# Kernel tuning notes

Measured on AMD Instinct MI355X. Metric: run time of the kernel, lower is better.

## Reference

```python
import jax, jax.numpy as jnp
import numpy as np

DECAY = 0.99
EPS = 1e-06


def setup_inputs() -> dict:
    key = jax.random.key(0)
    k1, k2, k3 = jax.random.split(key, 3)
    B, S, D, K = 8, 8192, 256, 2048
    x = jax.random.normal(k1, (B, S, D), dtype=jnp.float32)
    embed = jax.random.normal(k2, (K, D), dtype=jnp.float32)
    cluster_size = jnp.ones((K,), dtype=jnp.float32)
    embed_avg = jax.random.normal(k3, (K, D), dtype=jnp.float32)
    return {"x": x, "embed": embed, "cluster_size": cluster_size, "embed_avg": embed_avg}


def reference(x, embed, cluster_size, embed_avg):
    # x: [B, S, D]; embed/embed_avg: [K, D]; cluster_size: [K]
    B, S, D = x.shape
    K = embed.shape[0]
    xf = x.reshape(-1, D)  # [N, D]
    dist = (
        jnp.sum(xf * xf, axis=1, keepdims=True)
        - 2.0 * (xf @ embed.T)
        + jnp.sum(embed * embed, axis=1)
    )
    embed_ind_flat = jnp.argmin(dist, axis=-1)  # [N]
    quantize = embed[embed_ind_flat].reshape(B, S, D)
    embed_ind = embed_ind_flat.reshape(B, S)

    # EMA updates (training branch). one_hot.sum(0) == per-code counts,
    # one_hot.T @ x == per-code feature sums; use segment_sum (no NxK one-hot).
    counts = jax.ops.segment_sum(
        jnp.ones((B * S,), dtype=jnp.float32), embed_ind_flat, num_segments=K
    )
    embed_sum = jax.ops.segment_sum(xf, embed_ind_flat, num_segments=K)  # [K, D]
    new_cluster_size = cluster_size * DECAY + (1.0 - DECAY) * counts
    new_embed_avg = embed_avg * DECAY + (1.0 - DECAY) * embed_sum
    total = new_cluster_size.sum()
    smoothed = (new_cluster_size + EPS) / (total + EPS * K) * total  # laplace smoothing
    new_embed = new_embed_avg / smoothed[:, None]
    return quantize, embed_ind, new_cluster_size, new_embed_avg, new_embed
```

## Files before the change

### kernel.cpp

```cpp
#include <hip/hip_runtime.h>
#include <hip/hip_fp16.h>
#include <float.h>

#define DECAY 0.99f
#define OMD   0.01f
#define EPSF  1e-6f

constexpr int Bb = 8, Ss = 8192, Dd = 256, Kk = 2048;
constexpr int Nn = Bb * Ss;

constexpr long OUT_QUANT = 0;
constexpr long OUT_IND   = (long)Nn * Dd;
constexpr long OUT_NCS   = OUT_IND + Nn;
constexpr long OUT_NEA   = OUT_NCS + Kk;
constexpr long OUT_NE    = OUT_NEA + (long)Kk * Dd;

constexpr long WS_COUNTS = 0;
constexpr long WS_TOTAL  = 2048;
constexpr long WS_EE     = 2112;
constexpr long WS_BIG    = 4160;
constexpr int  PARTS     = 8;
constexpr int  CODES     = 8;

typedef __attribute__((ext_vector_type(8))) short short8;
typedef __attribute__((ext_vector_type(8))) _Float16 half8;
typedef __attribute__((ext_vector_type(4))) float floatx4;

#define WINDOW 0.5f

__device__ __forceinline__ ushort f2h(float v)
{
    __half h = __float2half(v);
    return *(ushort*)&h;
}

__global__ __launch_bounds__(256) void convert_e_kernel(
    const float* __restrict__ embed, ushort* __restrict__ e_h,
    float* __restrict__ ee, int* __restrict__ qbase)
{
    if (blockIdx.x == 0 && threadIdx.x == 0) qbase[0] = 0;
    int row  = blockIdx.x * 4 + (threadIdx.x >> 6);
    int lane = threadIdx.x & 63;
    long base = (long)row * Dd + lane * 4;
    float4 v = *(const float4*)&embed[base];
    float s = v.x * v.x + v.y * v.y + v.z * v.z + v.w * v.w;
    ushort4 h;
    h.x = f2h(v.x); h.y = f2h(v.y); h.z = f2h(v.z); h.w = f2h(v.w);
    *(ushort4*)&e_h[base] = h;
    #pragma unroll
    for (int off = 32; off >= 1; off >>= 1)
        s += __shfl_xor(s, off, 64);
    if (lane == 0) ee[row] = s;
}

__global__ __attribute__((amdgpu_waves_per_eu(2, 2))) __launch_bounds__(256)
void pass1_kernel(
    const float* __restrict__ x, const ushort* __restrict__ e_h,
    const float* __restrict__ embed, const float* __restrict__ ee,
    float* __restrict__ ind_out, float* __restrict__ quant,
    int* __restrict__ qbase)
{
    __shared__ __attribute__((aligned(16))) ushort as[64 * 256];
    __shared__ float redv[4][64];
    __shared__ float red2[4][64];
    __shared__ int   redi[4][64];

    const int tid  = threadIdx.x;
    const int lane = tid & 63;
    const int quad = lane >> 4;
    const int l15  = lane & 15;
    const int w    = tid >> 6;
    const long row0 = (long)blockIdx.x * 64;

    #pragma unroll
    for (int i = 0; i < 16; ++i) {
        int li = i * 256 + tid;
        int r  = li >> 6;
        int c  = (li & 63) * 4;
        float4 v = *(const float4*)&x[row0 * Dd + (long)li * 4];
        ushort4 h;
        h.x = f2h(v.x); h.y = f2h(v.y); h.z = f2h(v.z); h.w = f2h(v.w);
        int slot = (c >> 3) ^ (r & 7);
        *(ushort4*)&as[r * 256 + slot * 8 + (c & 7)] = h;
    }
    __syncthreads();

    float bestv[16], best2v[16];
    int   besti[16];
    #pragma unroll
    for (int i = 0; i < 16; ++i) { bestv[i] = FLT_MAX; best2v[i] = FLT_MAX; besti[i] = 0; }

    for (int ct = 0; ct < Kk / 128; ++ct) {
        floatx4 acc[4][2];
        #pragma unroll
        for (int rt = 0; rt < 4; ++rt)
            #pragma unroll
            for (int jt = 0; jt < 2; ++jt)
                acc[rt][jt] = (floatx4){0.f, 0.f, 0.f, 0.f};

        const int cbase = ct * 128 + w * 32 + l15;

        #pragma unroll
        for (int ks = 0; ks < 8; ++ks) {
            half8 af[4];
            #pragma unroll
            for (int rt = 0; rt < 4; ++rt) {
                int chunk = ks * 4 + quad;
                af[rt] = *(const half8*)&as[(rt * 16 + l15) * 256 +
                                            ((chunk ^ (l15 & 7)) << 3)];
            }
            #pragma unroll
            for (int jt = 0; jt < 2; ++jt) {
                const ushort* bp = &e_h[((long)(cbase + jt * 16) << 8) +
                                        ks * 32 + quad * 8];
                half8 bf = *(const half8*)bp;
                #pragma unroll
                for (int rt = 0; rt < 4; ++rt)
                    acc[rt][jt] = __builtin_amdgcn_mfma_f32_16x16x32_f16(
                        af[rt], bf, acc[rt][jt], 0, 0, 0);
            }
        }

        #pragma unroll
        for (int jt = 0; jt < 2; ++jt) {
            int c = ct * 128 + w * 32 + jt * 16 + l15;
            float eec = ee[c];
            #pragma unroll
            for (int rt = 0; rt < 4; ++rt) {
                #pragma unroll
                for (int reg = 0; reg < 4; ++reg) {
                    float s = eec - 2.0f * acc[rt][jt][reg];
                    int slot = rt * 4 + reg;
                    if (s < bestv[slot]) {
                        best2v[slot] = bestv[slot];
                        bestv[slot] = s; besti[slot] = c;
                    } else {
                        best2v[slot] = fminf(best2v[slot], s);
                    }
                }
            }
        }
    }

    #pragma unroll
    for (int slot = 0; slot < 16; ++slot) {
        float bv = bestv[slot]; int bi = besti[slot]; float b2 = best2v[slot];
        #pragma unroll
        for (int off = 8; off >= 1; off >>= 1) {
            float ov  = __shfl_xor(bv, off, 16);
            int   oi  = __shfl_xor(bi, off, 16);
            float ov2 = __shfl_xor(b2, off, 16);
            float nm2 = fminf(fminf(b2, ov2), fmaxf(bv, ov));
            if (ov < bv) { bv = ov; bi = oi; }
            b2 = nm2;
        }
        bestv[slot] = bv; besti[slot] = bi; best2v[slot] = b2;
    }

    if (l15 == 0) {
        #pragma unroll
        for (int rt = 0; rt < 4; ++rt)
            #pragma unroll
            for (int reg = 0; reg < 4; ++reg) {
                int rloc = rt * 16 + quad * 4 + reg;
                int slot = rt * 4 + reg;
                redv[w][rloc] = bestv[slot];
                red2[w][rloc] = best2v[slot];
                redi[w][rloc] = besti[slot];
            }
    }
    __syncthreads();

    if (tid < 64) {
        float v[4], s2[4]; int ix[4];
        #pragma unroll
        for (int p = 0; p < 4; ++p) {
            v[p] = redv[p][tid]; s2[p] = red2[p][tid]; ix[p] = redi[p][tid];
        }
        float m1 = v[0]; int mi = ix[0]; int arg = 0;
        #pragma unroll
        for (int p = 1; p < 4; ++p)
            if (v[p] < m1) { m1 = v[p]; mi = ix[p]; arg = p; }
        float m2 = FLT_MAX;
        #pragma unroll
        for (int p = 0; p < 4; ++p) {
            m2 = fminf(m2, s2[p]);
            if (p != arg) m2 = fminf(m2, v[p]);
        }
        long rowAbs = row0 + tid;
        ind_out[rowAbs] = (float)mi;
        redi[0][tid] = mi;
        if (m2 - m1 <= WINDOW) {
            int q = atomicAdd(qbase, 1);
            qbase[1 + q] = (int)rowAbs;
        }
    }
    __syncthreads();

    #pragma unroll
    for (int rr = 0; rr < 16; ++rr) {
        int row = w * 16 + rr;
        int idx = redi[0][row];
        float4 ev = *(const float4*)&embed[(long)idx * Dd + lane * 4];
        *(float4*)&quant[(row0 + row) * Dd + lane * 4] = ev;
    }
}

constexpr int RB = 8;
__global__ __launch_bounds__(256) void pass2_kernel(
    const float* __restrict__ x, const float* __restrict__ embed,
    const float* __restrict__ ee, const int* __restrict__ qbase,
    float* __restrict__ ind_out, float* __restrict__ quant)
{
    __shared__ float xs[RB][256];
    __shared__ float sv[RB][256];
    __shared__ int   si[RB][256];
    const int tid = threadIdx.x;
    const int count = qbase[0];

    for (int q0 = blockIdx.x * RB; q0 < count; q0 += gridDim.x * RB) {
        const int nr = (count - q0 < RB) ? (count - q0) : RB;
        __syncthreads();
        for (int r = 0; r < nr; ++r)
            xs[r][tid] = x[(long)qbase[1 + q0 + r] * Dd + tid];
        __syncthreads();

        float bv[RB]; int bi[RB];
        #pragma unroll
        for (int r = 0; r < RB; ++r) { bv[r] = FLT_MAX; bi[r] = 0; }

        for (int i = 0; i < Kk / 256; ++i) {
            const int c = i * 256 + tid;
            const float4* er = (const float4*)&embed[(long)c * Dd];
            float dot[RB];
            #pragma unroll
            for (int r = 0; r < RB; ++r) dot[r] = 0.0f;
            for (int d = 0; d < Dd / 4; ++d) {
                float4 e4 = er[d];
                #pragma unroll
                for (int r = 0; r < RB; ++r) {
                    float4 x4 = *(const float4*)&xs[r][d * 4];
                    dot[r] += e4.x * x4.x + e4.y * x4.y + e4.z * x4.z + e4.w * x4.w;
                }
            }
            float eec = ee[c];
            #pragma unroll
            for (int r = 0; r < RB; ++r) {
                float s = eec - 2.0f * dot[r];
                if (s < bv[r]) { bv[r] = s; bi[r] = c; }
            }
        }

        #pragma unroll
        for (int r = 0; r < RB; ++r) { sv[r][tid] = bv[r]; si[r][tid] = bi[r]; }
        __syncthreads();
        for (int off = 128; off >= 1; off >>= 1) {
            if (tid < off) {
                #pragma unroll
                for (int r = 0; r < RB; ++r) {
                    float v2 = sv[r][tid + off]; int i2 = si[r][tid + off];
                    if (v2 < sv[r][tid] || (v2 == sv[r][tid] && i2 < si[r][tid])) {
                        sv[r][tid] = v2; si[r][tid] = i2;
                    }
                }
            }
            __syncthreads();
        }
        if (tid < nr)
            ind_out[qbase[1 + q0 + tid]] = (float)si[tid][0];
        for (int r = 0; r < nr; ++r) {
            int code = si[r][0];
            long row = qbase[1 + q0 + r];
            quant[row * Dd + tid] = embed[(long)code * Dd + tid];
        }
        __syncthreads();
    }
}

template <int USE_ATOMIC>
__global__ __launch_bounds__(256) void segsum_kernel(
    const float* __restrict__ x, const float* __restrict__ ind_f,
    float* __restrict__ dst, float* __restrict__ counts)
{
    __shared__ float part[CODES][4][256];
    __shared__ float cnt_l[CODES][4];
    const int tid  = threadIdx.x;
    const int w    = tid >> 6;
    const int lane = tid & 63;
    const int k0   = (blockIdx.x >> 3) * CODES;
    const int s    = blockIdx.x & 7;

    constexpr int STRIP = Nn / PARTS;
    constexpr int WAVE_ROWS = STRIP / 4;
    const int base0 = s * STRIP + w * WAVE_ROWS;

    float4 acc[CODES];
    int    cnt[CODES];
    #pragma unroll
    for (int c = 0; c < CODES; ++c) { acc[c] = (float4){0.f,0.f,0.f,0.f}; cnt[c] = 0; }

    for (int win = 0; win < WAVE_ROWS; win += 64) {
        int idx = (int)ind_f[base0 + win + lane];
        unsigned rel = (unsigned)(idx - k0);
        unsigned long long m = __ballot(rel < (unsigned)CODES);
        while (m) {
            int l = __ffsll((unsigned long long)m) - 1;
            m &= m - 1;
            int code = __shfl((int)rel, l, 64);
            long row = base0 + win + l;
            float4 v = *(const float4*)&x[row * Dd + lane * 4];
            switch (code) {
                case 0: acc[0].x+=v.x; acc[0].y+=v.y; acc[0].z+=v.z; acc[0].w+=v.w; cnt[0]++; break;
                case 1: acc[1].x+=v.x; acc[1].y+=v.y; acc[1].z+=v.z; acc[1].w+=v.w; cnt[1]++; break;
                case 2: acc[2].x+=v.x; acc[2].y+=v.y; acc[2].z+=v.z; acc[2].w+=v.w; cnt[2]++; break;
                case 3: acc[3].x+=v.x; acc[3].y+=v.y; acc[3].z+=v.z; acc[3].w+=v.w; cnt[3]++; break;
                case 4: acc[4].x+=v.x; acc[4].y+=v.y; acc[4].z+=v.z; acc[4].w+=v.w; cnt[4]++; break;
                case 5: acc[5].x+=v.x; acc[5].y+=v.y; acc[5].z+=v.z; acc[5].w+=v.w; cnt[5]++; break;
                case 6: acc[6].x+=v.x; acc[6].y+=v.y; acc[6].z+=v.z; acc[6].w+=v.w; cnt[6]++; break;
                case 7: acc[7].x+=v.x; acc[7].y+=v.y; acc[7].z+=v.z; acc[7].w+=v.w; cnt[7]++; break;
            }
        }
    }

    #pragma unroll
    for (int c = 0; c < CODES; ++c) {
        *(float4*)&part[c][w][lane * 4] = acc[c];
        if (lane == 0) cnt_l[c][w] = (float)cnt[c];
    }
    __syncthreads();

    #pragma unroll
    for (int c = 0; c < CODES; ++c) {
        float sum = part[c][0][tid] + part[c][1][tid] + part[c][2][tid] + part[c][3][tid];
        if (USE_ATOMIC) {
            if (sum != 0.0f) atomicAdd(&dst[(long)(k0 + c) * Dd + tid], sum);
        } else {
            dst[((long)s * Kk + (k0 + c)) * Dd + tid] = sum;
        }
    }
    if (tid < CODES)
        atomicAdd(&counts[k0 + tid],
                  cnt_l[tid][0] + cnt_l[tid][1] + cnt_l[tid][2] + cnt_l[tid][3]);
}

__global__ __launch_bounds__(256) void ema_cs_kernel(
    const float* __restrict__ cs, const float* __restrict__ counts,
    float* __restrict__ ncs, float* __restrict__ total_ws)
{
    __shared__ float red[256];
    int tid = threadIdx.x;
    float s = 0.0f;
    #pragma unroll
    for (int i = 0; i < 8; ++i) {
        int k = tid + i * 256;
        float v = cs[k] * DECAY + OMD * counts[k];
        ncs[k] = v;
        s += v;
    }
    red[tid] = s;
    __syncthreads();
    #pragma unroll
    for (int off = 128; off >= 1; off >>= 1) {
        if (tid < off) red[tid] += red[tid + off];
        __syncthreads();
    }
    if (tid == 0) total_ws[0] = red[0];
}

__global__ __launch_bounds__(256) void nea_ne_kernel(
    const float* __restrict__ ea, const float* __restrict__ partials,
    int nparts, const float* __restrict__ ncs, const float* __restrict__ total_ws,
    float* __restrict__ nea, float* __restrict__ ne)
{
    long g = ((long)blockIdx.x * 256 + threadIdx.x) * 4;
    int  k = (int)(g >> 8);
    int  d = (int)(g & 255);

    float4 sv = {0.f, 0.f, 0.f, 0.f};
    for (int p = 0; p < nparts; ++p) {
        float4 pv = *(const float4*)&partials[((long)p * Kk + k) * Dd + d];
        sv.x += pv.x; sv.y += pv.y; sv.z += pv.z; sv.w += pv.w;
    }

    float4 av = *(const float4*)&ea[g];
    float4 out_nea;
    out_nea.x = av.x * DECAY + OMD * sv.x;
    out_nea.y = av.y * DECAY + OMD * sv.y;
    out_nea.z = av.z * DECAY + OMD * sv.z;
    out_nea.w = av.w * DECAY + OMD * sv.w;
    *(float4*)&nea[g] = out_nea;

    float total = total_ws[0];
    float sm = (ncs[k] + EPSF) / (total + EPSF * (float)Kk) * total;
    float inv = 1.0f / sm;
    float4 out_ne;
    out_ne.x = out_nea.x * inv;
    out_ne.y = out_nea.y * inv;
    out_ne.z = out_nea.z * inv;
    out_ne.w = out_nea.w * inv;
    *(float4*)&ne[g] = out_ne;
}

extern "C" void kernel_launch(void* const* d_in, const int* in_sizes, int n_in,
                              void* d_out, int out_size, void* d_ws, size_t ws_size,
                              hipStream_t stream)
{
    const float* x     = (const float*)d_in[0];
    const float* embed = (const float*)d_in[1];
    const float* cs    = (const float*)d_in[2];
    const float* ea    = (const float*)d_in[3];

    float* out   = (float*)d_out;
    float* quant = out + OUT_QUANT;
    float* ind_f = out + OUT_IND;
    float* ncs   = out + OUT_NCS;
    float* nea   = out + OUT_NEA;
    float* ne    = out + OUT_NE;

    float* ws     = (float*)d_ws;
    float* counts = ws + WS_COUNTS;
    float* total  = ws + WS_TOTAL;
    float* ee     = ws + WS_EE;
    float* big    = ws + WS_BIG;

    ushort* e_h = (ushort*)(out + OUT_NEA);
    int*    qb  = (int*)(out + OUT_NE);

    const size_t need_partials =
        (size_t)(WS_BIG + (long)PARTS * Kk * Dd) * sizeof(float) + 1024;
    const bool use_ws_partials = ws_size >= need_partials;

    hipMemsetAsync(counts, 0, Kk * sizeof(float), stream);
    if (!use_ws_partials)
        hipMemsetAsync(big, 0, (size_t)Kk * Dd * sizeof(float), stream);

    convert_e_kernel<<<Kk / 4, 256, 0, stream>>>(embed, e_h, ee, qb);
    pass1_kernel<<<Nn / 64, 256, 0, stream>>>(x, e_h, embed, ee, ind_f, quant, qb);
    pass2_kernel<<<512, 256, 0, stream>>>(x, embed, ee, qb, ind_f, quant);
    if (use_ws_partials)
        segsum_kernel<0><<<(Kk / CODES) * PARTS, 256, 0, stream>>>(x, ind_f, big, counts);
    else
        segsum_kernel<1><<<(Kk / CODES) * PARTS, 256, 0, stream>>>(x, ind_f, big, counts);
    ema_cs_kernel<<<1, 256, 0, stream>>>(cs, counts, ncs, total);
    nea_ne_kernel<<<(Kk * Dd / 4) / 256, 256, 0, stream>>>(
        ea, big, use_ws_partials ? PARTS : 1, ncs, total, nea, ne);
}
```

Before: 447.6 us.

## Keep x fragments in registers and split codebook across waves in pass1

Pass1 drops the shared-memory staging of x. Each wave now loads its 32 rows of x straight into half8 register fragments, and the codebook is split in two halves across wave pairs, with a two-way reduction at the end. The wave occupancy hint goes from 2 to 3 per EU. Pass2's fallback distance loop is restructured so that four codes are processed per thread at once, which reuses the shared x loads across codes. The aim is to cut LDS traffic and sync and raise occupancy, at the cost of more register pressure and more redundant global reads of codebook fragments per wave.

```diff
diff --git a/kernel.cpp b/kernel.cpp
--- a/kernel.cpp
+++ b/kernel.cpp
@@ -53,97 +53,98 @@
     if (lane == 0) ee[row] = s;
 }
 
-__global__ __attribute__((amdgpu_waves_per_eu(2, 2))) __launch_bounds__(256)
+__global__ __attribute__((amdgpu_waves_per_eu(3, 3))) __launch_bounds__(256)
 void pass1_kernel(
     const float* __restrict__ x, const ushort* __restrict__ e_h,
     const float* __restrict__ embed, const float* __restrict__ ee,
     float* __restrict__ ind_out, float* __restrict__ quant,
     int* __restrict__ qbase)
 {
-    __shared__ __attribute__((aligned(16))) ushort as[64 * 256];
-    __shared__ float redv[4][64];
-    __shared__ float red2[4][64];
-    __shared__ int   redi[4][64];
+    __shared__ float redv[2][64];
+    __shared__ float red2[2][64];
+    __shared__ int   redi[2][64];
+    __shared__ int   idxs[64];
 
     const int tid  = threadIdx.x;
     const int lane = tid & 63;
     const int quad = lane >> 4;
     const int l15  = lane & 15;
     const int w    = tid >> 6;
-    const long row0 = (long)blockIdx.x * 64;
-
-    #pragma unroll
-    for (int i = 0; i < 16; ++i) {
-        int li = i * 256 + tid;
-        int r  = li >> 6;
-        int c  = (li & 63) * 4;
-        float4 v = *(const float4*)&x[row0 * Dd + (long)li * 4];
-        ushort4 h;
-        h.x = f2h(v.x); h.y = f2h(v.y); h.z = f2h(v.z); h.w = f2h(v.w);
-        int slot = (c >> 3) ^ (r & 7);
-        *(ushort4*)&as[r * 256 + slot * 8 + (c & 7)] = h;
-    }
-    __syncthreads();
-
-    float bestv[16], best2v[16];
-    int   besti[16];
-    #pragma unroll
-    for (int i = 0; i < 16; ++i) { bestv[i] = FLT_MAX; best2v[i] = FLT_MAX; besti[i] = 0; }
-
-    for (int ct = 0; ct < Kk / 128; ++ct) {
-        floatx4 acc[4][2];
-        #pragma unroll
-        for (int rt = 0; rt < 4; ++rt)
-            #pragma unroll
-            for (int jt = 0; jt < 2; ++jt)
-                acc[rt][jt] = (floatx4){0.f, 0.f, 0.f, 0.f};
-
-        const int cbase = ct * 128 + w * 32 + l15;
-
+    const int part = w & 1;
+    const int rg   = w >> 1;
+    const long row0  = (long)blockIdx.x * 64;
+    const long row0w = row0 + rg * 32;
+
+    half8 af0[8], af1[8];
+    {
+        const long ra0 = (row0w + l15) << 8;
+        const long ra1 = (row0w + 16 + l15) << 8;
         #pragma unroll
         for (int ks = 0; ks < 8; ++ks) {
-            half8 af[4];
-            #pragma unroll
-            for (int rt = 0; rt < 4; ++rt) {
-                int chunk = ks * 4 + quad;
-                af[rt] = *(const half8*)&as[(rt * 16 + l15) * 256 +
-                                            ((chunk ^ (l15 & 7)) << 3)];
-            }
-            #pragma unroll
-            for (int jt = 0; jt < 2; ++jt) {
-                const ushort* bp = &e_h[((long)(cbase + jt * 16) << 8) +
-                                        ks * 32 + quad * 8];
-                half8 bf = *(const half8*)bp;
-                #pragma unroll
-                for (int rt = 0; rt < 4; ++rt)
-                    acc[rt][jt] = __builtin_amdgcn_mfma_f32_16x16x32_f16(
-                        af[rt], bf, acc[rt][jt], 0, 0, 0);
-            }
-        }
-
-        #pragma unroll
-        for (int jt = 0; jt < 2; ++jt) {
-            int c = ct * 128 + w * 32 + jt * 16 + l15;
-            float eec = ee[c];
-            #pragma unroll
-            for (int rt = 0; rt < 4; ++rt) {
-                #pragma unroll
-                for (int reg = 0; reg < 4; ++reg) {
-                    float s = eec - 2.0f * acc[rt][jt][reg];
-                    int slot = rt * 4 + reg;
-                    if (s < bestv[slot]) {
-                        best2v[slot] = bestv[slot];
-                        bestv[slot] = s; besti[slot] = c;
-                    } else {
-                        best2v[slot] = fminf(best2v[slot], s);
-                    }
-                }
-            }
-        }
-    }
-
-    #pragma unroll
-    for (int slot = 0; slot < 16; ++slot) {
+            const int off = ks * 32 + quad * 8;
+            float4 a = *(const float4*)&x[ra0 + off];
+            float4 b = *(const float4*)&x[ra0 + off + 4];
+            half8 h;
+            h[0] = (_Float16)a.x; h[1] = (_Float16)a.y;
+            h[2] = (_Float16)a.z; h[3] = (_Float16)a.w;
+            h[4] = (_Float16)b.x; h[5] = (_Float16)b.y;
+            h[6] = (_Float16)b.z; h[7] = (_Float16)b.w;
+            af0[ks] = h;
+            float4 c = *(const float4*)&x[ra1 + off];
+            float4 d = *(const float4*)&x[ra1 + off + 4];
+            half8 g;
+            g[0] = (_Float16)c.x; g[1] = (_Float16)c.y;
+            g[2] = (_Float16)c.z; g[3] = (_Float16)c.w;
+            g[4] = (_Float16)d.x; g[5] = (_Float16)d.y;
+            g[6] = (_Float16)d.z; g[7] = (_Float16)d.w;
+            af1[ks] = g;
+        }
+    }
+
+    float bestv[8], best2v[8];
+    int   besti[8];
+    #pragma unroll
+    for (int i = 0; i < 8; ++i) { bestv[i] = FLT_MAX; best2v[i] = FLT_MAX; besti[i] = 0; }
+
+    const ushort* bbase = e_h + (((long)part * 1024 + l15) << 8) + quad * 8;
+    const float*  eeb   = ee + part * 1024 + l15;
+
+    for (int ct = 0; ct < 64; ++ct) {
+        half8 bf[8];
+        #pragma unroll
+        for (int ks = 0; ks < 8; ++ks)
+            bf[ks] = *(const half8*)&bbase[ct * 4096 + ks * 32];
+        float eec = eeb[ct * 16];
+
+        floatx4 acc0 = (floatx4){0.f, 0.f, 0.f, 0.f};
+        floatx4 acc1 = (floatx4){0.f, 0.f, 0.f, 0.f};
+        #pragma unroll
+        for (int ks = 0; ks < 8; ++ks) {
+            acc0 = __builtin_amdgcn_mfma_f32_16x16x32_f16(af0[ks], bf[ks], acc0, 0, 0, 0);
+            acc1 = __builtin_amdgcn_mfma_f32_16x16x32_f16(af1[ks], bf[ks], acc1, 0, 0, 0);
+        }
+
+        const int cc = part * 1024 + ct * 16 + l15;
+        #pragma unroll
+        for (int reg = 0; reg < 4; ++reg) {
+            float s = fmaf(-2.0f, acc0[reg], eec);
+            if (s < bestv[reg]) {
+                best2v[reg] = bestv[reg]; bestv[reg] = s; besti[reg] = cc;
+            } else {
+                best2v[reg] = fminf(best2v[reg], s);
+            }
+            float t = fmaf(-2.0f, acc1[reg], eec);
+            const int sl = 4 + reg;
+            if (t < bestv[sl]) {
+                best2v[sl] = bestv[sl]; bestv[sl] = t; besti[sl] = cc;
+            } else {
+                best2v[sl] = fminf(best2v[sl], t);
+            }
+        }
+    }
+
+    #pragma unroll
+    for (int slot = 0; slot < 8; ++slot) {
         float bv = bestv[slot]; int bi = besti[slot]; float b2 = best2v[slot];
         #pragma unroll
         for (int off = 8; off >= 1; off >>= 1) {
@@ -159,37 +160,27 @@
 
     if (l15 == 0) {
         #pragma unroll
-        for (int rt = 0; rt < 4; ++rt)
+        for (int rt = 0; rt < 2; ++rt)
             #pragma unroll
             for (int reg = 0; reg < 4; ++reg) {
-                int rloc = rt * 16 + quad * 4 + reg;
+                int r = rg * 32 + rt * 16 + quad * 4 + reg;
                 int slot = rt * 4 + reg;
-                redv[w][rloc] = bestv[slot];
-                red2[w][rloc] = best2v[slot];
-                redi[w][rloc] = besti[slot];
+                redv[part][r] = bestv[slot];
+                red2[part][r] = best2v[slot];
+                redi[part][r] = besti[slot];
             }
     }
     __syncthreads();
 
     if (tid < 64) {
-        float v[4], s2[4]; int ix[4];
-        #pragma unroll
-        for (int p = 0; p < 4; ++p) {
-            v[p] = redv[p][tid]; s2[p] = red2[p][tid]; ix[p] = redi[p][tid];
-        }
-        float m1 = v[0]; int mi = ix[0]; int arg = 0;
-        #pragma unroll
-        for (int p = 1; p < 4; ++p)
-            if (v[p] < m1) { m1 = v[p]; mi = ix[p]; arg = p; }
-        float m2 = FLT_MAX;
-        #pragma unroll
-        for (int p = 0; p < 4; ++p) {
-            m2 = fminf(m2, s2[p]);
-            if (p != arg) m2 = fminf(m2, v[p]);
-        }
+        float v0 = redv[0][tid], v1 = redv[1][tid];
+        float s0 = red2[0][tid], s1 = red2[1][tid];
+        float m1, m2; int mi;
+        if (v0 <= v1) { m1 = v0; mi = redi[0][tid]; m2 = fminf(fminf(s0, s1), v1); }
+        else          { m1 = v1; mi = redi[1][tid]; m2 = fminf(fminf(s0, s1), v0); }
         long rowAbs = row0 + tid;
         ind_out[rowAbs] = (float)mi;
-        redi[0][tid] = mi;
+        idxs[tid] = mi;
         if (m2 - m1 <= WINDOW) {
             int q = atomicAdd(qbase, 1);
             qbase[1 + q] = (int)rowAbs;
@@ -199,10 +190,10 @@
 
     #pragma unroll
     for (int rr = 0; rr < 16; ++rr) {
-        int row = w * 16 + rr;
-        int idx = redi[0][row];
+        int r = w * 16 + rr;
+        int idx = idxs[r];
         float4 ev = *(const float4*)&embed[(long)idx * Dd + lane * 4];
-        *(float4*)&quant[(row0 + row) * Dd + lane * 4] = ev;
+        *(float4*)&quant[(row0 + r) * Dd + lane * 4] = ev;
     }
 }
 
@@ -229,25 +220,38 @@
         #pragma unroll
         for (int r = 0; r < RB; ++r) { bv[r] = FLT_MAX; bi[r] = 0; }
 
-        for (int i = 0; i < Kk / 256; ++i) {
-            const int c = i * 256 + tid;
-            const float4* er = (const float4*)&embed[(long)c * Dd];
-            float dot[RB];
+        #pragma unroll
+        for (int g = 0; g < 2; ++g) {
+            float dot[RB][4];
             #pragma unroll
-            for (int r = 0; r < RB; ++r) dot[r] = 0.0f;
+            for (int r = 0; r < RB; ++r)
+                #pragma unroll
+                for (int j = 0; j < 4; ++j) dot[r][j] = 0.0f;
+
             for (int d = 0; d < Dd / 4; ++d) {
-                float4 e4 = er[d];
+                float4 xv[RB];
+                #pragma unroll
+                for (int r = 0; r < RB; ++r)
+                    xv[r] = *(const float4*)&xs[r][d * 4];
+                #pragma unroll
+                for (int j = 0; j < 4; ++j) {
+                    const int c = g * 1024 + j * 256 + tid;
+                    float4 e4 = *(const float4*)&embed[(long)c * Dd + d * 4];
+                    #pragma unroll
+                    for (int r = 0; r < RB; ++r)
+                        dot[r][j] += e4.x * xv[r].x + e4.y * xv[r].y +
+                                     e4.z * xv[r].z + e4.w * xv[r].w;
+                }
+            }
+            #pragma unroll
+            for (int j = 0; j < 4; ++j) {
+                const int c = g * 1024 + j * 256 + tid;
+                float eec = ee[c];
                 #pragma unroll
                 for (int r = 0; r < RB; ++r) {
-                    float4 x4 = *(const float4*)&xs[r][d * 4];
-                    dot[r] += e4.x * x4.x + e4.y * x4.y + e4.z * x4.z + e4.w * x4.w;
+                    float s = eec - 2.0f * dot[r][j];
+                    if (s < bv[r]) { bv[r] = s; bi[r] = c; }
                 }
-            }
-            float eec = ee[c];
-            #pragma unroll
-            for (int r = 0; r < RB; ++r) {
-                float s = eec - 2.0f * dot[r];
-                if (s < bv[r]) { bv[r] = s; bi[r] = c; }
             }
         }
 
```

New measurement: 657.6 us. 1.47x slower.

## Coalesce pass2 embed loads via quad-split dot products and shuffle-based argmin

Applied to the files above, without the earlier changes.

The fallback re-check kernel now assigns each code to four consecutive lanes, which split the 256-wide dot product and combine partials with xor shuffles. Adjacent lanes therefore read contiguous embed memory instead of striding by a whole row. The block-wide shared-memory argmin tree with many barriers becomes an in-wave shuffle reduction plus a small cross-wave merge. This adds shuffle work per code, and tie-breaking order still depends on the lowest index.

```diff
diff --git a/kernel.cpp b/kernel.cpp
--- a/kernel.cpp
+++ b/kernel.cpp
@@ -213,9 +213,14 @@
     float* __restrict__ ind_out, float* __restrict__ quant)
 {
     __shared__ float xs[RB][256];
-    __shared__ float sv[RB][256];
-    __shared__ int   si[RB][256];
-    const int tid = threadIdx.x;
+    __shared__ float mv[4][RB];
+    __shared__ int   mi[4][RB];
+    __shared__ int   fin[RB];
+    const int tid  = threadIdx.x;
+    const int w    = tid >> 6;
+    const int lane = tid & 63;
+    const int cq   = lane >> 2;
+    const int ph   = lane & 3;
     const int count = qbase[0];
 
     for (int q0 = blockIdx.x * RB; q0 < count; q0 += gridDim.x * RB) {
@@ -229,51 +234,67 @@
         #pragma unroll
         for (int r = 0; r < RB; ++r) { bv[r] = FLT_MAX; bi[r] = 0; }
 
-        for (int i = 0; i < Kk / 256; ++i) {
-            const int c = i * 256 + tid;
-            const float4* er = (const float4*)&embed[(long)c * Dd];
-            float dot[RB];
-            #pragma unroll
-            for (int r = 0; r < RB; ++r) dot[r] = 0.0f;
-            for (int d = 0; d < Dd / 4; ++d) {
-                float4 e4 = er[d];
+        for (int ch = 0; ch < 32; ++ch) {
+            const int c = w * 512 + ch * 16 + cq;
+            const float4* ep = (const float4*)&embed[(long)c * Dd + ph * 4];
+            float acc[RB];
+            #pragma unroll
+            for (int r = 0; r < RB; ++r) acc[r] = 0.0f;
+
+            #pragma unroll
+            for (int d0 = 0; d0 < 16; ++d0) {
+                float4 e4 = ep[d0 * 4];
                 #pragma unroll
                 for (int r = 0; r < RB; ++r) {
-                    float4 x4 = *(const float4*)&xs[r][d * 4];
-                    dot[r] += e4.x * x4.x + e4.y * x4.y + e4.z * x4.z + e4.w * x4.w;
+                    float4 x4 = *(const float4*)&xs[r][d0 * 16 + ph * 4];
+                    acc[r] += e4.x * x4.x + e4.y * x4.y +
+                              e4.z * x4.z + e4.w * x4.w;
                 }
             }
+            #pragma unroll
+            for (int r = 0; r < RB; ++r) {
+                acc[r] += __shfl_xor(acc[r], 1, 4);
+                acc[r] += __shfl_xor(acc[r], 2, 4);
+            }
             float eec = ee[c];
             #pragma unroll
             for (int r = 0; r < RB; ++r) {
-                float s = eec - 2.0f * dot[r];
+                float s = eec - 2.0f * acc[r];
                 if (s < bv[r]) { bv[r] = s; bi[r] = c; }
             }
         }
 
         #pragma unroll
-        for (int r = 0; r < RB; ++r) { sv[r][tid] = bv[r]; si[r][tid] = bi[r]; }
+        for (int r = 0; r < RB; ++r) {
+            #pragma unroll
+            for (int off = 4; off <= 32; off <<= 1) {
+                float ov = __shfl_xor(bv[r], off, 64);
+                int   oi = __shfl_xor(bi[r], off, 64);
+                if (ov < bv[r] || (ov == bv[r] && oi < bi[r])) {
+                    bv[r] = ov; bi[r] = oi;
+                }
+            }
+        }
+        if (lane == 0) {
+            #pragma unroll
+            for (int r = 0; r < RB; ++r) { mv[w][r] = bv[r]; mi[w][r] = bi[r]; }
+        }
         __syncthreads();
-        for (int off = 128; off >= 1; off >>= 1) {
-            if (tid < off) {
-                #pragma unroll
-                for (int r = 0; r < RB; ++r) {
-                    float v2 = sv[r][tid + off]; int i2 = si[r][tid + off];
-                    if (v2 < sv[r][tid] || (v2 == sv[r][tid] && i2 < si[r][tid])) {
-                        sv[r][tid] = v2; si[r][tid] = i2;
-                    }
-                }
-            }
-            __syncthreads();
-        }
-        if (tid < nr)
-            ind_out[qbase[1 + q0 + tid]] = (float)si[tid][0];
-        for (int r = 0; r < nr; ++r) {
-            int code = si[r][0];
-            long row = qbase[1 + q0 + r];
-            quant[row * Dd + tid] = embed[(long)code * Dd + tid];
+
+        if (tid < RB) {
+            float best = mv[0][tid]; int bidx = mi[0][tid];
+            #pragma unroll
+            for (int ww = 1; ww < 4; ++ww) {
+                float v = mv[ww][tid]; int i = mi[ww][tid];
+                if (v < best || (v == best && i < bidx)) { best = v; bidx = i; }
+            }
+            fin[tid] = bidx;
+            if (tid < nr) ind_out[qbase[1 + q0 + tid]] = (float)bidx;
         }
         __syncthreads();
+
+        for (int r = 0; r < nr; ++r)
+            quant[(long)qbase[1 + q0 + r] * Dd + tid] = embed[(long)fin[r] * Dd + tid];
     }
 }
 
```

New measurement: 732.7 us. +63.7%, slower.
